# Optimization experiments

Hardware: AMD Instinct MI355X
Metric: run time of the kernel (lower is better)

The kernel has to match this reference:

```python
import jax, jax.numpy as jnp
import numpy as np

D = 1024
B, LQ, LK = 8, 2048, 2048
NEG = -1e9


def setup_inputs() -> dict:
    key = jax.random.key(0)
    ks = jax.random.split(key, 8)
    query = jax.random.normal(ks[0], (B, LQ, D), dtype=jnp.float32)
    k_in = jax.random.normal(ks[1], (B, LK, D), dtype=jnp.float32)
    value = jax.random.normal(ks[2], (B, LK, D), dtype=jnp.float32)
    mask = jax.random.randint(ks[3], (B, LK), 0, 2, dtype=jnp.int32)
    s = 1.0 / np.sqrt(D)
    Wq_w = jax.random.normal(ks[4], (D, D), dtype=jnp.float32) * s
    Wq_b = jnp.zeros((D,), dtype=jnp.float32)
    Wk_w = jax.random.normal(ks[5], (D, D), dtype=jnp.float32) * s
    Wk_b = jnp.zeros((D,), dtype=jnp.float32)
    return {"query": query, "key": k_in, "value": value, "mask": mask,
            "Wq_w": Wq_w, "Wq_b": Wq_b, "Wk_w": Wk_w, "Wk_b": Wk_b}


def reference(query, key, value, mask, Wq_w, Wq_b, Wk_w, Wk_b):
    # Linear projections (torch Linear: x @ W.T + b)
    q = jnp.einsum('bld,ed->ble', query, Wq_w) + Wq_b  # [B, Lq, D]
    k = jnp.einsum('bld,ed->ble', key, Wk_w) + Wk_b    # [B, Lk, D]
    scale = 1.0 / jnp.sqrt(jnp.asarray(D, dtype=q.dtype))
    aw = jnp.einsum('bqd,bkd->bqk', q, k) * scale      # [B, Lq, Lk]
    # custom multiplicative + additive masking: mask -> [B, 1, Lk]
    m = mask.astype(aw.dtype)[:, None, :]
    aw = aw * m
    aw = jnp.where(m == 0, jnp.asarray(NEG, dtype=aw.dtype), aw)
    attn = jax.nn.softmax(aw, axis=-1)
    return jnp.einsum('bqk,bkd->bqd', attn, value)     # [B, Lq, D]
```

## Files before the change

kernel.cpp:

```cpp
#include <hip/hip_runtime.h>

typedef __bf16 bf16;
typedef __bf16 bf16x8 __attribute__((ext_vector_type(8)));
typedef float f32x4 __attribute__((ext_vector_type(4)));
typedef float f32x16 __attribute__((ext_vector_type(16)));

__device__ __forceinline__ void gl_lds16(const bf16* g, bf16* l) {
  __builtin_amdgcn_global_load_lds(
      (__attribute__((address_space(1))) void*)g,
      (__attribute__((address_space(3))) void*)l, 16, 0, 0);
}

__global__ __launch_bounds__(256) void cvt_f32_bf16(
    const float* __restrict__ src, bf16* __restrict__ dst, int n8) {
  int i = blockIdx.x * 256 + threadIdx.x;
  if (i >= n8) return;
  const float4* s4 = (const float4*)src;
  float4 a = s4[2 * i], b = s4[2 * i + 1];
  bf16x8 o = {(bf16)a.x, (bf16)a.y, (bf16)a.z, (bf16)a.w,
              (bf16)b.x, (bf16)b.y, (bf16)b.z, (bf16)b.w};
  *(bf16x8*)(dst + (size_t)i * 8) = o;
}

__global__ __launch_bounds__(256) void transpose_v(
    const float* __restrict__ V, bf16* __restrict__ VT) {
  int b = blockIdx.z;
  const float* Vb = V + (size_t)b * 2048 * 1024;
  bf16* Tb = VT + (size_t)b * 1024 * 2048;
  __shared__ float tile[32][33];
  int tx = threadIdx.x, ty = threadIdx.y;
  int x = blockIdx.x * 32 + tx;
  int yb = blockIdx.y * 32;
#pragma unroll
  for (int j = 0; j < 4; j++)
    tile[ty + j * 8][tx] = Vb[(size_t)(yb + ty + j * 8) * 1024 + x];
  __syncthreads();
  int xo = yb + tx;
#pragma unroll
  for (int j = 0; j < 4; j++)
    Tb[(size_t)(blockIdx.x * 32 + ty + j * 8) * 2048 + xo] =
        (bf16)tile[tx][ty + j * 8];
}

template <int MODE, int ZMAP>
__global__ __launch_bounds__(512, 2) void gemm256(
    const bf16* __restrict__ A, const bf16* __restrict__ Bm,
    void* __restrict__ Cv, const float* __restrict__ bias,
    const int* __restrict__ mask, int M, int N, int K,
    long long sA, long long sB, long long sC) {
  int b, m0, n0;
  if constexpr (ZMAP == 1) {
    const int L = (blockIdx.z * gridDim.y + blockIdx.y) * gridDim.x +
                  blockIdx.x;
    b = L & 7;
    const int J = L >> 3;
    m0 = (J / gridDim.x) * 256;
    n0 = (J % gridDim.x) * 256;
  } else {
    b = blockIdx.z;
    const int nx = gridDim.x, nwg = nx * gridDim.y;
    const int orig = blockIdx.y * nx + blockIdx.x;
    const int swz = (orig & 7) * (nwg >> 3) + (orig >> 3);
    m0 = (swz / nx) * 256;
    n0 = (swz % nx) * 256;
  }
  const bf16* Ab = A + (long long)b * sA;
  const bf16* Bb = Bm + (long long)b * sB;

  __shared__ __align__(16) bf16 lds[2][2][256 * 64];

  const int tid = threadIdx.x, w = tid >> 6, lane = tid & 63;
  const int wr = w >> 2, wc = w & 3;
  const int fr = lane & 31;
  const int fh = lane >> 5;
  const int key = (fr & 7) ^ (((fr >> 3) & 3) << 1);
  const bf16* Aq = Ab + (long long)m0 * K;
  const bf16* Bq = Bb + (long long)n0 * K;

  f32x16 acc[4][2];
#pragma unroll
  for (int i = 0; i < 4; i++)
#pragma unroll
    for (int j = 0; j < 2; j++)
#pragma unroll
      for (int r = 0; r < 16; r++) acc[i][j][r] = 0.f;

  const int srow = lane >> 3;
  const int sgsw = (((lane & 7) ^ srow ^ ((w & 3) << 1)) * 8);
  auto stage_tile = [&](int t) {
    const int buf = t & 1;
    const long long gc = (long long)t * 64 + sgsw;
    const int r0 = w * 8 + srow;
#pragma unroll
    for (int p = 0; p < 4; p++) {
      const long long r = p * 64 + r0;
      const int dbase = (p * 64 + w * 8) * 64;
      gl_lds16(Aq + r * K + gc, &lds[buf][0][dbase]);
      gl_lds16(Bq + r * K + gc, &lds[buf][1][dbase]);
    }
  };

  auto compute_tile = [&](int buf) {
    const bf16* la = &lds[buf][0][0];
    const bf16* lb = &lds[buf][1][0];
#pragma unroll
    for (int kk = 0; kk < 4; kk++) {
      const int slot = ((kk * 2 + fh) ^ key) * 8;
      bf16x8 af[4], bfr[2];
#pragma unroll
      for (int mi = 0; mi < 4; mi++)
        af[mi] = *(const bf16x8*)&la[(wr * 128 + mi * 32 + fr) * 64 + slot];
#pragma unroll
      for (int ni = 0; ni < 2; ni++)
        bfr[ni] = *(const bf16x8*)&lb[(wc * 64 + ni * 32 + fr) * 64 + slot];
      __builtin_amdgcn_s_setprio(1);
#pragma unroll
      for (int mi = 0; mi < 4; mi++)
#pragma unroll
        for (int ni = 0; ni < 2; ni++)
          acc[mi][ni] = __builtin_amdgcn_mfma_f32_32x32x16_bf16(
              af[mi], bfr[ni], acc[mi][ni], 0, 0, 0);
      __builtin_amdgcn_s_setprio(0);
    }
  };

  const int NT = K >> 6;
  stage_tile(0);
  for (int t = 0; t < NT; ++t) {
    if (t + 1 < NT) {
      stage_tile(t + 1);
      asm volatile("s_waitcnt vmcnt(8)" ::: "memory");
    } else {
      asm volatile("s_waitcnt vmcnt(0)" ::: "memory");
    }
    __builtin_amdgcn_s_barrier();
    compute_tile(t & 1);
    __builtin_amdgcn_s_barrier();
  }

  const int ecol = lane & 31, er4 = (lane >> 5) * 4;
  if constexpr (MODE == 0) {
    bf16* C = (bf16*)Cv;
#pragma unroll
    for (int ni = 0; ni < 2; ni++) {
      int col = n0 + wc * 64 + ni * 32 + ecol;
      float bv = bias[col];
#pragma unroll
      for (int mi = 0; mi < 4; mi++)
#pragma unroll
        for (int r = 0; r < 16; r++) {
          int row = m0 + wr * 128 + mi * 32 + er4 + (r & 3) + 8 * (r >> 2);
          C[(long long)row * N + col] = (bf16)(acc[mi][ni][r] + bv);
        }
    }
  } else if constexpr (MODE == 1) {
    bf16* C = (bf16*)Cv + (long long)b * sC;
    const int* mb = mask + b * 2048;
#pragma unroll
    for (int ni = 0; ni < 2; ni++) {
      int col = n0 + wc * 64 + ni * 32 + ecol;
      bool keep = mb[col] != 0;
#pragma unroll
      for (int mi = 0; mi < 4; mi++)
#pragma unroll
        for (int r = 0; r < 16; r++) {
          int row = m0 + wr * 128 + mi * 32 + er4 + (r & 3) + 8 * (r >> 2);
          C[(long long)row * N + col] =
              keep ? (bf16)(acc[mi][ni][r] * 0.03125f) : (bf16)(-1e9f);
        }
    }
  } else {
    float* C = (float*)Cv + (long long)b * sC;
#pragma unroll
    for (int ni = 0; ni < 2; ni++) {
      int col = n0 + wc * 64 + ni * 32 + ecol;
#pragma unroll
      for (int mi = 0; mi < 4; mi++)
#pragma unroll
        for (int r = 0; r < 16; r++) {
          int row = m0 + wr * 128 + mi * 32 + er4 + (r & 3) + 8 * (r >> 2);
          C[(long long)row * N + col] = acc[mi][ni][r];
        }
    }
  }
}

__global__ __launch_bounds__(256) void softmax_rows(
    const bf16* __restrict__ S, bf16* __restrict__ P) {
  long long row = blockIdx.x;
  const bf16x8* src = (const bf16x8*)(S + row * 2048);
  int tid = threadIdx.x, w = tid >> 6, lane = tid & 63;
  bf16x8 v = src[tid];
  float f[8];
#pragma unroll
  for (int i = 0; i < 8; i++) f[i] = (float)v[i];
  float m = f[0];
#pragma unroll
  for (int i = 1; i < 8; i++) m = fmaxf(m, f[i]);
#pragma unroll
  for (int off = 32; off; off >>= 1) m = fmaxf(m, __shfl_xor(m, off, 64));
  __shared__ float redm[4], reds[4];
  if (lane == 0) redm[w] = m;
  __syncthreads();
  m = fmaxf(fmaxf(redm[0], redm[1]), fmaxf(redm[2], redm[3]));
  float e[8], s = 0.f;
#pragma unroll
  for (int i = 0; i < 8; i++) {
    e[i] = __expf(f[i] - m);
    s += e[i];
  }
#pragma unroll
  for (int off = 32; off; off >>= 1) s += __shfl_xor(s, off, 64);
  if (lane == 0) reds[w] = s;
  __syncthreads();
  s = reds[0] + reds[1] + reds[2] + reds[3];
  float inv = 1.0f / s;
  bf16x8 o;
#pragma unroll
  for (int i = 0; i < 8; i++) o[i] = (bf16)(e[i] * inv);
  *(bf16x8*)(P + row * 2048 + tid * 8) = o;
}

extern "C" void kernel_launch(void* const* d_in, const int* in_sizes, int n_in,
                              void* d_out, int out_size, void* d_ws,
                              size_t ws_size, hipStream_t stream) {
  const float* query = (const float*)d_in[0];
  const float* key_in = (const float*)d_in[1];
  const float* value = (const float*)d_in[2];
  const int* mask = (const int*)d_in[3];
  const float* Wq_w = (const float*)d_in[4];
  const float* Wq_b = (const float*)d_in[5];
  const float* Wk_w = (const float*)d_in[6];
  const float* Wk_b = (const float*)d_in[7];
  float* out = (float*)d_out;

  const size_t MB = 1ull << 20;
  char* base = (char*)d_ws;
  bf16* qx = (bf16*)(base + 0 * MB);
  bf16* kx = (bf16*)(base + 32 * MB);
  bf16* wq = (bf16*)(base + 64 * MB);
  bf16* wk = (bf16*)(base + 66 * MB);
  bf16* S = (bf16*)(base + 0 * MB);
  bf16* qp = (bf16*)(base + 128 * MB);
  bf16* kp = (bf16*)(base + 160 * MB);
  bf16* P = (bf16*)(base + 128 * MB);
  bf16* vt = (bf16*)(base + 192 * MB);

  cvt_f32_bf16<<<8192, 256, 0, stream>>>(query, qx, 2097152);
  cvt_f32_bf16<<<8192, 256, 0, stream>>>(key_in, kx, 2097152);
  cvt_f32_bf16<<<512, 256, 0, stream>>>(Wq_w, wq, 131072);
  cvt_f32_bf16<<<512, 256, 0, stream>>>(Wk_w, wk, 131072);
  transpose_v<<<dim3(32, 64, 8), dim3(32, 8), 0, stream>>>(value, vt);

  gemm256<0, 0><<<dim3(4, 64, 1), 512, 0, stream>>>(
      qx, wq, qp, Wq_b, nullptr, 16384, 1024, 1024, 0, 0, 0);
  gemm256<0, 0><<<dim3(4, 64, 1), 512, 0, stream>>>(
      kx, wk, kp, Wk_b, nullptr, 16384, 1024, 1024, 0, 0, 0);
  gemm256<1, 1><<<dim3(8, 8, 8), 512, 0, stream>>>(
      qp, kp, S, nullptr, mask, 2048, 2048, 1024, 2048LL * 1024,
      2048LL * 1024, 2048LL * 2048);
  softmax_rows<<<16384, 256, 0, stream>>>(S, P);
  gemm256<2, 1><<<dim3(4, 8, 8), 512, 0, stream>>>(
      P, vt, out, nullptr, nullptr, 2048, 1024, 2048, 2048LL * 2048,
      1024LL * 2048, 2048LL * 1024);
}
```

Before: 487.7 us.

## Split GEMM tile into quadrants and interleave half-tile prefetch with compute

Restructures the GEMM main loop so each 256x256 block tile is computed as four 128x128 quadrants. Each wave now owns a 64x32 sub-block per quadrant instead of a 128x64 block. Global-to-LDS loads for the next k-tile are issued in four half-matrix pieces, one per quadrant, with finer vmcnt waits and barriers. The goal is to spread memory traffic evenly across the MFMA work and hide load latency better, at the cost of four times as many barriers per k-tile.

```diff
diff --git a/kernel.cpp b/kernel.cpp
--- a/kernel.cpp
+++ b/kernel.cpp
@@ -87,99 +87,119 @@
 
   const int srow = lane >> 3;
   const int sgsw = (((lane & 7) ^ srow ^ ((w & 3) << 1)) * 8);
-  auto stage_tile = [&](int t) {
+  auto stage_half = [&](int t, int mat, int half) {
     const int buf = t & 1;
     const long long gc = (long long)t * 64 + sgsw;
-    const int r0 = w * 8 + srow;
-#pragma unroll
-    for (int p = 0; p < 4; p++) {
-      const long long r = p * 64 + r0;
-      const int dbase = (p * 64 + w * 8) * 64;
-      gl_lds16(Aq + r * K + gc, &lds[buf][0][dbase]);
-      gl_lds16(Bq + r * K + gc, &lds[buf][1][dbase]);
+    const bf16* src = mat ? Bq : Aq;
+#pragma unroll
+    for (int j = 0; j < 2; j++) {
+      const long long r = half * 128 + j * 64 + w * 8 + srow;
+      const int dbase = (half * 128 + j * 64 + w * 8) * 64;
+      gl_lds16(src + r * K + gc, &lds[buf][mat][dbase]);
     }
   };
 
-  auto compute_tile = [&](int buf) {
+  const int NT = K >> 6;
+  stage_half(0, 0, 0);
+  stage_half(0, 1, 0);
+  stage_half(0, 1, 1);
+  stage_half(0, 0, 1);
+  asm volatile("s_waitcnt vmcnt(4)" ::: "memory");
+  __builtin_amdgcn_s_barrier();
+
+  for (int t = 0; t < NT; ++t) {
+    if (t == NT - 1) {
+      asm volatile("s_waitcnt vmcnt(0)" ::: "memory");
+      __builtin_amdgcn_s_barrier();
+    }
+    const int buf = t & 1;
     const bf16* la = &lds[buf][0][0];
     const bf16* lb = &lds[buf][1][0];
 #pragma unroll
-    for (int kk = 0; kk < 4; kk++) {
-      const int slot = ((kk * 2 + fh) ^ key) * 8;
-      bf16x8 af[4], bfr[2];
-#pragma unroll
-      for (int mi = 0; mi < 4; mi++)
-        af[mi] = *(const bf16x8*)&la[(wr * 128 + mi * 32 + fr) * 64 + slot];
-#pragma unroll
-      for (int ni = 0; ni < 2; ni++)
-        bfr[ni] = *(const bf16x8*)&lb[(wc * 64 + ni * 32 + fr) * 64 + slot];
+    for (int q = 0; q < 4; q++) {
+      const int mh = q >> 1, nh = q & 1;
+      bf16x8 afv[2][4], bfv[4];
+#pragma unroll
+      for (int kk = 0; kk < 4; kk++) {
+        const int slot = ((kk * 2 + fh) ^ key) * 8;
+#pragma unroll
+        for (int mi2 = 0; mi2 < 2; mi2++)
+          afv[mi2][kk] = *(const bf16x8*)&la
+              [(mh * 128 + wr * 64 + mi2 * 32 + fr) * 64 + slot];
+        bfv[kk] =
+            *(const bf16x8*)&lb[(nh * 128 + wc * 32 + fr) * 64 + slot];
+      }
+      if (t + 1 < NT) {
+        constexpr int smat[4] = {0, 1, 1, 0};
+        constexpr int shalf[4] = {0, 0, 1, 1};
+        stage_half(t + 1, smat[q], shalf[q]);
+      }
+      __builtin_amdgcn_s_barrier();
+      asm volatile("s_waitcnt lgkmcnt(0)" ::: "memory");
+      __builtin_amdgcn_sched_barrier(0);
       __builtin_amdgcn_s_setprio(1);
 #pragma unroll
-      for (int mi = 0; mi < 4; mi++)
-#pragma unroll
-        for (int ni = 0; ni < 2; ni++)
-          acc[mi][ni] = __builtin_amdgcn_mfma_f32_32x32x16_bf16(
-              af[mi], bfr[ni], acc[mi][ni], 0, 0, 0);
+      for (int kk = 0; kk < 4; kk++)
+#pragma unroll
+        for (int mi2 = 0; mi2 < 2; mi2++)
+          acc[q][mi2] = __builtin_amdgcn_mfma_f32_32x32x16_bf16(
+              afv[mi2][kk], bfv[kk], acc[q][mi2], 0, 0, 0);
       __builtin_amdgcn_s_setprio(0);
-    }
-  };
-
-  const int NT = K >> 6;
-  stage_tile(0);
-  for (int t = 0; t < NT; ++t) {
-    if (t + 1 < NT) {
-      stage_tile(t + 1);
-      asm volatile("s_waitcnt vmcnt(8)" ::: "memory");
-    } else {
-      asm volatile("s_waitcnt vmcnt(0)" ::: "memory");
-    }
-    __builtin_amdgcn_s_barrier();
-    compute_tile(t & 1);
-    __builtin_amdgcn_s_barrier();
+      if (t + 1 < NT) {
+        if (q == 2)
+          asm volatile("s_waitcnt vmcnt(6)" ::: "memory");
+        else
+          asm volatile("s_waitcnt vmcnt(4)" ::: "memory");
+      }
+      __builtin_amdgcn_s_barrier();
+    }
   }
 
   const int ecol = lane & 31, er4 = (lane >> 5) * 4;
   if constexpr (MODE == 0) {
     bf16* C = (bf16*)Cv;
 #pragma unroll
-    for (int ni = 0; ni < 2; ni++) {
-      int col = n0 + wc * 64 + ni * 32 + ecol;
+    for (int q = 0; q < 4; q++) {
+      int col = n0 + (q & 1) * 128 + wc * 32 + ecol;
       float bv = bias[col];
 #pragma unroll
-      for (int mi = 0; mi < 4; mi++)
+      for (int mi2 = 0; mi2 < 2; mi2++)
 #pragma unroll
         for (int r = 0; r < 16; r++) {
-          int row = m0 + wr * 128 + mi * 32 + er4 + (r & 3) + 8 * (r >> 2);
-          C[(long long)row * N + col] = (bf16)(acc[mi][ni][r] + bv);
+          int row = m0 + (q >> 1) * 128 + wr * 64 + mi2 * 32 + er4 +
+                    (r & 3) + 8 * (r >> 2);
+          C[(long long)row * N + col] = (bf16)(acc[q][mi2][r] + bv);
         }
     }
   } else if constexpr (MODE == 1) {
     bf16* C = (bf16*)Cv + (long long)b * sC;
     const int* mb = mask + b * 2048;
 #pragma unroll
-    for (int ni = 0; ni < 2; ni++) {
-      int col = n0 + wc * 64 + ni * 32 + ecol;
+    for (int q = 0; q < 4; q++) {
+      int col = n0 + (q & 1) * 128 + wc * 32 + ecol;
       bool keep = mb[col] != 0;
 #pragma unroll
-      for (int mi = 0; mi < 4; mi++)
+      for (int mi2 = 0; mi2 < 2; mi2++)
 #pragma unroll
         for (int r = 0; r < 16; r++) {
-          int row = m0 + wr * 128 + mi * 32 + er4 + (r & 3) + 8 * (r >> 2);
+          int row = m0 + (q >> 1) * 128 + wr * 64 + mi2 * 32 + er4 +
+                    (r & 3) + 8 * (r >> 2);
           C[(long long)row * N + col] =
-              keep ? (bf16)(acc[mi][ni][r] * 0.03125f) : (bf16)(-1e9f);
+              keep ? (bf16)(acc[q][mi2][r] * 0.03125f) : (bf16)(-1e9f);
         }
     }
   } else {
     float* C = (float*)Cv + (long long)b * sC;
 #pragma unroll
-    for (int ni = 0; ni < 2; ni++) {
-      int col = n0 + wc * 64 + ni * 32 + ecol;
-#pragma unroll
-      for (int mi = 0; mi < 4; mi++)
+    for (int q = 0; q < 4; q++) {
+      int col = n0 + (q & 1) * 128 + wc * 32 + ecol;
+#pragma unroll
+      for (int mi2 = 0; mi2 < 2; mi2++)
 #pragma unroll
         for (int r = 0; r < 16; r++) {
-          int row = m0 + wr * 128 + mi * 32 + er4 + (r & 3) + 8 * (r >> 2);
-          C[(long long)row * N + col] = acc[mi][ni][r];
+          int row = m0 + (q >> 1) * 128 + wr * 64 + mi2 * 32 + er4 +
+                    (r & 3) + 8 * (r >> 2);
+          C[(long long)row * N + col] = acc[q][mi2][r];
         }
     }
   }
```

Result: slower. 529.1 us (+8.5%).
